# Kernel tuning notes

Measured on AMD Instinct MI355X. Metric: run time of the kernel, lower is better.

Reference implementation:

```python
import jax, jax.numpy as jnp
import numpy as np
import math

# dims: batch, tgt_len, img_feat, wordvec, heads, vocab, layers, ffn
N, T, D, W, H, V, L, FF = 8, 512, 1024, 512, 4, 32000, 2, 2048
NULL = 0  # padding_idx -> zero embedding row


def _pos_encoding(max_len, dim):
    pos = jnp.arange(max_len, dtype=jnp.float32)[:, None]
    j = jnp.arange(dim)[None, :]
    je = (j - (j % 2)).astype(jnp.float32)
    ang = pos * jnp.power(10000.0, -je / dim)
    return jnp.where(j % 2 == 0, jnp.sin(ang), jnp.cos(ang))  # (max_len, dim)


def setup_inputs() -> dict:
    key = jax.random.key(0)
    ks = iter(jax.random.split(key, 80))

    def nrm(shape):
        return jax.random.normal(next(ks), shape, jnp.float32) * 0.02

    inp = {}
    inp["features"] = jax.random.normal(next(ks), (N, D), jnp.float32)
    inp["captions"] = jax.random.randint(next(ks), (N, T), 0, V)
    emb = nrm((V, W)).at[NULL].set(0.0)  # padding_idx row zeroed
    inp["emb"] = emb
    inp["pe"] = _pos_encoding(T, W)
    inp["vis_w"] = nrm((D, W)); inp["vis_b"] = jnp.zeros((W,), jnp.float32)
    for p in ["sa", "ca"]:
        for q in ["q", "k", "v", "o"]:
            inp[f"{p}_w{q}"] = nrm((L, W, W))
            inp[f"{p}_b{q}"] = jnp.zeros((L, W), jnp.float32)
    inp["ff1_w"] = nrm((L, W, FF)); inp["ff1_b"] = jnp.zeros((L, FF), jnp.float32)
    inp["ff2_w"] = nrm((L, FF, W)); inp["ff2_b"] = jnp.zeros((L, W), jnp.float32)
    for i in (1, 2, 3):
        inp[f"ln{i}_w"] = jnp.ones((L, W), jnp.float32)
        inp[f"ln{i}_b"] = jnp.zeros((L, W), jnp.float32)
    inp["out_w"] = nrm((W, V)); inp["out_b"] = jnp.zeros((V,), jnp.float32)
    return inp


def _layer_norm(x, w, b):
    m = x.mean(-1, keepdims=True)
    v = ((x - m) ** 2).mean(-1, keepdims=True)
    return (x - m) / jnp.sqrt(v + 1e-5) * w + b


def _mha(qx, kx, vx, wq, bq, wk, bk, wv, bv, wo, bo, mask):
    n, s, e = qx.shape
    t = kx.shape[1]
    d = e // H
    q = (qx @ wq + bq).reshape(n, s, H, d)
    k = (kx @ wk + bk).reshape(n, t, H, d)
    v = (vx @ wv + bv).reshape(n, t, H, d)
    a = jnp.einsum("nshd,nthd->nhst", q, k) / math.sqrt(d)  # (N,H,S,T)
    if mask is not None:
        a = jnp.where(mask, a, -jnp.inf)
    e_ = jax.nn.softmax(a, axis=-1)
    y = jnp.einsum("nhst,nthd->nshd", e_, v).reshape(n, s, e)
    return y @ wo + bo


def reference(features, captions, emb, pe, vis_w, vis_b,
              sa_wq, sa_bq, sa_wk, sa_bk, sa_wv, sa_bv, sa_wo, sa_bo,
              ca_wq, ca_bq, ca_wk, ca_bk, ca_wv, ca_bv, ca_wo, ca_bo,
              ff1_w, ff1_b, ff2_w, ff2_b,
              ln1_w, ln1_b, ln2_w, ln2_b, ln3_w, ln3_b, out_w, out_b):
    memory = (features @ vis_w + vis_b)[:, None, :]  # (N,1,W)
    t_len = captions.shape[1]
    x = emb[captions] + pe[None, :t_len, :]  # (N,T,W)
    mask = jnp.tril(jnp.ones((t_len, t_len), bool))  # causal tgt_mask
    for l in range(L):
        t2 = _mha(x, x, x, sa_wq[l], sa_bq[l], sa_wk[l], sa_bk[l],
                  sa_wv[l], sa_bv[l], sa_wo[l], sa_bo[l], mask)
        x = _layer_norm(x + t2, ln1_w[l], ln1_b[l])
        t2 = _mha(x, memory, memory, ca_wq[l], ca_bq[l], ca_wk[l], ca_bk[l],
                  ca_wv[l], ca_bv[l], ca_wo[l], ca_bo[l], None)
        x = _layer_norm(x + t2, ln2_w[l], ln2_b[l])
        t2 = jax.nn.relu(x @ ff1_w[l] + ff1_b[l]) @ ff2_w[l] + ff2_b[l]
        x = _layer_norm(x + t2, ln3_w[l], ln3_b[l])
    return x @ out_w + out_b  # (N,T,V)
```

## Files before the change

### kernel.cpp

```cpp
#include <hip/hip_runtime.h>
#include <math.h>

#define WDIM   512
#define TLEN   512
#define NBATCH 8
#define NHEADS 4
#define DHEAD  128
#define VOCAB  32000
#define NLAY   2
#define FFDIM  2048
#define DFEAT  1024
#define NT     (NBATCH * TLEN)
#define QKVW   (3 * WDIM)

typedef unsigned short u16;
typedef __attribute__((ext_vector_type(8))) short bf16x8;
typedef __attribute__((ext_vector_type(4))) float f32x4;

__device__ inline u16 f2bf(float f) {
    union { float f; unsigned u; } v; v.f = f;
    unsigned r = v.u + 0x7fffu + ((v.u >> 16) & 1u);
    return (u16)(r >> 16);
}
__device__ inline u16 to_bf(float f) { return f2bf(f); }
__device__ inline u16 to_bf(u16 v)  { return v; }

__global__ __launch_bounds__(256)
void cvt_kernel(const float* __restrict__ s, u16* __restrict__ d, int n)
{
    int i = blockIdx.x * 256 + threadIdx.x;
    if (i < n) d[i] = f2bf(s[i]);
}

__global__ __launch_bounds__(256)
void concat_bias_kernel(const float* __restrict__ bq, const float* __restrict__ bk,
                        const float* __restrict__ bv, float* __restrict__ dst)
{
    int i = blockIdx.x * 256 + threadIdx.x;
    if (i >= NLAY * QKVW) return;
    int l = i / QKVW, j = i - l * QKVW;
    float v = (j < WDIM) ? bq[l * WDIM + j]
            : (j < 2 * WDIM) ? bk[l * WDIM + j - WDIM]
            : bv[l * WDIM + j - 2 * WDIM];
    dst[i] = v;
}

template<typename T>
__global__ __launch_bounds__(256)
void transpose_cvt_kernel(const T* __restrict__ src, int lds_, long ssn, long ssh,
                          u16* __restrict__ dst, int ldd, long dsn, long dsh,
                          int HH)
{
    int z = blockIdx.z;
    int zn = z / HH, zh = z - zn * HH;
    src += (long)zn * ssn + (long)zh * ssh;
    dst += (long)zn * dsn + (long)zh * dsh;
    __shared__ T tile[32][33];
    int n0 = blockIdx.x * 32, k0 = blockIdx.y * 32;
    int tx = threadIdx.x & 31, ty = threadIdx.x >> 5;
    #pragma unroll
    for (int i = 0; i < 32; i += 8)
        tile[ty + i][tx] = src[(long)(k0 + ty + i) * lds_ + n0 + tx];
    __syncthreads();
    #pragma unroll
    for (int i = 0; i < 32; i += 8)
        dst[(long)(n0 + ty + i) * ldd + k0 + tx] = to_bf(tile[tx][ty + i]);
}

__global__ __launch_bounds__(128)
void embed_kernel(const int* __restrict__ captions, const float* __restrict__ emb,
                  const float* __restrict__ pe, float* __restrict__ x, u16* __restrict__ xb)
{
    int r = blockIdx.x;
    int t = r % TLEN;
    int cap = captions[r];
    const float4* e4 = (const float4*)(emb + (long)cap * WDIM);
    const float4* p4 = (const float4*)(pe + (long)t * WDIM);
    float4 a = e4[threadIdx.x], b = p4[threadIdx.x];
    float4 o = make_float4(a.x + b.x, a.y + b.y, a.z + b.z, a.w + b.w);
    ((float4*)(x + (long)r * WDIM))[threadIdx.x] = o;
    ushort4 ob = make_ushort4(f2bf(o.x), f2bf(o.y), f2bf(o.z), f2bf(o.w));
    ((ushort4*)(xb + (long)r * WDIM))[threadIdx.x] = ob;
}

#define GBM 128
#define GBN 128
#define GBK 32

template<int RELU, int NTST, int CAUSAL>
__global__ __launch_bounds__(256)
void mfma_gemm_kernel(const u16* __restrict__ A, int lda, long sAn, long sAh,
                      const u16* __restrict__ B, int ldb, long sBn, long sBh,
                      float* __restrict__ C, u16* __restrict__ Cb, int ldc, long sCn, long sCh,
                      const float* __restrict__ bias,
                      int M, int N, int K, int HH, float alpha)
{
    int z = blockIdx.z;
    int zn = z / HH, zh = z - zn * HH;
    A += (long)zn * sAn + (long)zh * sAh;
    B += (long)zn * sBn + (long)zh * sBh;
    long coff = (long)zn * sCn + (long)zh * sCh;

    int nwg  = gridDim.x * gridDim.y;
    int orig = blockIdx.y * gridDim.x + blockIdx.x;
    int q = nwg >> 3, r = nwg & 7, xcd = orig & 7, rest = orig >> 3;
    int nw = (xcd < r ? xcd * (q + 1) : r * (q + 1) + (xcd - r) * q) + rest;
    int bx = nw / gridDim.y, by = nw - bx * gridDim.y;
    int bm = by * GBM, bn = bx * GBN;

    if (CAUSAL && bn >= bm + GBM) return;

    __shared__ u16 smem[2 * GBM * GBK];
    u16* As = smem;
    u16* Bs = smem + GBM * GBK;

    int tid = threadIdx.x;
    int w = tid >> 6, lane = tid & 63;
    int wr = w >> 1, wc = w & 1;
    int lrow = lane & 15, kgrp = lane >> 4;

    f32x4 acc[4][4] = {};

    for (int k0 = 0; k0 < K; k0 += GBK) {
        #pragma unroll
        for (int i = 0; i < 2; i++) {
            int c = tid + i * 256;
            int row = c >> 2, ko = (c & 3) << 3;
            int gr = bm + row; if (gr >= M) gr = M - 1;
            const u16* src = A + (long)gr * lda + k0 + ko;
            u16* dst = &As[(size_t)(w * 64 + i * 256) * 8];
            __builtin_amdgcn_global_load_lds((const __attribute__((address_space(1))) void*)src,
                                             (__attribute__((address_space(3))) void*)dst, 16, 0, 0);
        }
        #pragma unroll
        for (int i = 0; i < 2; i++) {
            int c = tid + i * 256;
            int row = c >> 2, ko = (c & 3) << 3;
            const u16* src = B + (long)(bn + row) * ldb + k0 + ko;
            u16* dst = &Bs[(size_t)(w * 64 + i * 256) * 8];
            __builtin_amdgcn_global_load_lds((const __attribute__((address_space(1))) void*)src,
                                             (__attribute__((address_space(3))) void*)dst, 16, 0, 0);
        }
        __syncthreads();
        bf16x8 av[4], bv[4];
        #pragma unroll
        for (int m = 0; m < 4; m++)
            av[m] = *(const bf16x8*)&As[(wr * 64 + m * 16 + lrow) * GBK + kgrp * 8];
        #pragma unroll
        for (int n = 0; n < 4; n++)
            bv[n] = *(const bf16x8*)&Bs[(wc * 64 + n * 16 + lrow) * GBK + kgrp * 8];
        #pragma unroll
        for (int m = 0; m < 4; m++)
            #pragma unroll
            for (int n = 0; n < 4; n++)
                acc[m][n] = __builtin_amdgcn_mfma_f32_16x16x32_bf16(av[m], bv[n], acc[m][n], 0, 0, 0);
        __syncthreads();
    }

    if (NTST) {
        float* ls = (float*)smem;
        C += coff;
        #pragma unroll
        for (int pass = 0; pass < 4; pass++) {
            if (wr == (pass >> 1)) {
                #pragma unroll
                for (int m2 = 0; m2 < 2; m2++) {
                    int m = (pass & 1) * 2 + m2;
                    #pragma unroll
                    for (int n = 0; n < 4; n++) {
                        int gc = wc * 64 + n * 16 + lrow;
                        float bvv = bias ? bias[bn + gc] : 0.f;
                        #pragma unroll
                        for (int r2 = 0; r2 < 4; r2++) {
                            float v2 = acc[m][n][r2] * alpha + bvv;
                            if (RELU) v2 = fmaxf(v2, 0.f);
                            ls[(m2 * 16 + kgrp * 4 + r2) * 128 + gc] = v2;
                        }
                    }
                }
            }
            __syncthreads();
            #pragma unroll
            for (int i = 0; i < 4; i++) {
                int j = tid + i * 256;
                int row = j >> 5, cg = j & 31;
                int gr = bm + pass * 32 + row;
                if (gr < M) {
                    f32x4 v4 = *(const f32x4*)&ls[row * 128 + cg * 4];
                    __builtin_nontemporal_store(v4, (f32x4*)&C[(long)gr * ldc + bn + cg * 4]);
                }
            }
            __syncthreads();
        }
        return;
    }

    if (C)  C  += coff;
    if (Cb) Cb += coff;
    #pragma unroll
    for (int m = 0; m < 4; m++) {
        int rb = bm + wr * 64 + m * 16 + kgrp * 4;
        #pragma unroll
        for (int n = 0; n < 4; n++) {
            int gc = bn + wc * 64 + n * 16 + lrow;
            float bvv = bias ? bias[gc] : 0.f;
            #pragma unroll
            for (int r2 = 0; r2 < 4; r2++) {
                int gr = rb + r2;
                if (gr < M) {
                    float v2 = acc[m][n][r2] * alpha + bvv;
                    if (RELU) v2 = fmaxf(v2, 0.f);
                    if (C)  C[(long)gr * ldc + gc]  = v2;
                    if (Cb) Cb[(long)gr * ldc + gc] = f2bf(v2);
                }
            }
        }
    }
}

__global__ __launch_bounds__(256)
void softmax_causal_kernel(const float* __restrict__ scores, u16* __restrict__ pb)
{
    long row = blockIdx.x;
    int s = (int)(row % TLEN);
    const float* p = scores + row * TLEN;
    u16* o = pb + row * TLEN;
    int tid = threadIdx.x;
    float v0 = p[tid], v1 = p[tid + 256];
    bool m0 = (tid <= s), m1 = (tid + 256 <= s);
    __shared__ float red[256];
    float mx = fmaxf(m0 ? v0 : -INFINITY, m1 ? v1 : -INFINITY);
    red[tid] = mx; __syncthreads();
    for (int off = 128; off > 0; off >>= 1) {
        if (tid < off) red[tid] = fmaxf(red[tid], red[tid + off]);
        __syncthreads();
    }
    mx = red[0]; __syncthreads();
    float e0 = m0 ? expf(v0 - mx) : 0.f;
    float e1 = m1 ? expf(v1 - mx) : 0.f;
    red[tid] = e0 + e1; __syncthreads();
    for (int off = 128; off > 0; off >>= 1) {
        if (tid < off) red[tid] += red[tid + off];
        __syncthreads();
    }
    float inv = 1.f / red[0];
    o[tid]       = f2bf(e0 * inv);
    o[tid + 256] = f2bf(e1 * inv);
}

__global__ __launch_bounds__(256)
void add_ln_kernel(float* __restrict__ x, u16* __restrict__ xb,
                   const float* __restrict__ t2, long t2div,
                   const float* __restrict__ w, const float* __restrict__ b)
{
    long r = blockIdx.x;
    float* xr = x + r * WDIM;
    u16* xbr = xb + r * WDIM;
    const float* tr = t2 + (r / t2div) * WDIM;
    int tid = threadIdx.x;
    float v0 = xr[tid] + tr[tid];
    float v1 = xr[tid + 256] + tr[tid + 256];
    __shared__ float red[256];
    red[tid] = v0 + v1; __syncthreads();
    for (int off = 128; off > 0; off >>= 1) {
        if (tid < off) red[tid] += red[tid + off];
        __syncthreads();
    }
    float mean = red[0] * (1.f / WDIM); __syncthreads();
    float d0 = v0 - mean, d1 = v1 - mean;
    red[tid] = d0 * d0 + d1 * d1; __syncthreads();
    for (int off = 128; off > 0; off >>= 1) {
        if (tid < off) red[tid] += red[tid + off];
        __syncthreads();
    }
    float rstd = 1.f / sqrtf(red[0] * (1.f / WDIM) + 1e-5f);
    float o0 = d0 * rstd * w[tid] + b[tid];
    float o1 = d1 * rstd * w[tid + 256] + b[tid + 256];
    xr[tid] = o0;        xr[tid + 256] = o1;
    xbr[tid] = f2bf(o0); xbr[tid + 256] = f2bf(o1);
}

extern "C" void kernel_launch(void* const* d_in, const int* in_sizes, int n_in,
                              void* d_out, int out_size, void* d_ws, size_t ws_size,
                              hipStream_t stream)
{
    const float* features = (const float*)d_in[0];
    const int*   captions = (const int*)  d_in[1];
    const float* emb      = (const float*)d_in[2];
    const float* pe       = (const float*)d_in[3];
    const float* vis_w    = (const float*)d_in[4];
    const float* vis_b    = (const float*)d_in[5];
    const float* sa_wq    = (const float*)d_in[6];
    const float* sa_bq    = (const float*)d_in[7];
    const float* sa_wk    = (const float*)d_in[8];
    const float* sa_bk    = (const float*)d_in[9];
    const float* sa_wv    = (const float*)d_in[10];
    const float* sa_bv    = (const float*)d_in[11];
    const float* sa_wo    = (const float*)d_in[12];
    const float* sa_bo    = (const float*)d_in[13];
    const float* ca_wv    = (const float*)d_in[18];
    const float* ca_bv    = (const float*)d_in[19];
    const float* ca_wo    = (const float*)d_in[20];
    const float* ca_bo    = (const float*)d_in[21];
    const float* ff1_w    = (const float*)d_in[22];
    const float* ff1_b    = (const float*)d_in[23];
    const float* ff2_w    = (const float*)d_in[24];
    const float* ff2_b    = (const float*)d_in[25];
    const float* ln1_w    = (const float*)d_in[26];
    const float* ln1_b    = (const float*)d_in[27];
    const float* ln2_w    = (const float*)d_in[28];
    const float* ln2_b    = (const float*)d_in[29];
    const float* ln3_w    = (const float*)d_in[30];
    const float* ln3_b    = (const float*)d_in[31];
    const float* out_w    = (const float*)d_in[32];
    const float* out_b    = (const float*)d_in[33];

    char* p = (char*)d_ws;
    auto alloc = [&](size_t bytes) { char* r = p; p += (bytes + 255) & ~(size_t)255; return r; };
    float* x    = (float*)alloc((size_t)NT * WDIM * 4);
    float* t2   = (float*)alloc((size_t)NT * WDIM * 4);
    float* memb = (float*)alloc((size_t)NBATCH * WDIM * 4);
    float* cav  = (float*)alloc((size_t)NBATCH * WDIM * 4);
    char*  reg1 = alloc((size_t)NBATCH * NHEADS * TLEN * TLEN * 4);
    float* scores = (float*)reg1;
    u16*   yb     = (u16*)reg1;
    u16*   hb     = (u16*)reg1;
    u16* xb    = (u16*)alloc((size_t)NT * WDIM * 2);
    u16* qkvb  = (u16*)alloc((size_t)NT * QKVW * 2);
    u16* vtb   = (u16*)alloc((size_t)NT * WDIM * 2);
    u16* pb    = (u16*)alloc((size_t)NBATCH * NHEADS * TLEN * TLEN * 2);
    u16* featb = (u16*)alloc((size_t)NBATCH * DFEAT * 2);
    u16* membf = (u16*)alloc((size_t)NBATCH * WDIM * 2);
    u16* cvb   = (u16*)alloc((size_t)NBATCH * WDIM * 2);
    float* qkv_bias = (float*)alloc((size_t)NLAY * QKVW * 4);
    u16* vis_wT = (u16*)alloc((size_t)WDIM * DFEAT * 2);
    u16* qkvT   = (u16*)alloc((size_t)NLAY * QKVW * WDIM * 2);
    u16* sa_woT = (u16*)alloc((size_t)NLAY * WDIM * WDIM * 2);
    u16* ca_wvT = (u16*)alloc((size_t)NLAY * WDIM * WDIM * 2);
    u16* ca_woT = (u16*)alloc((size_t)NLAY * WDIM * WDIM * 2);
    u16* ff1T   = (u16*)alloc((size_t)NLAY * WDIM * FFDIM * 2);
    u16* ff2T   = (u16*)alloc((size_t)NLAY * FFDIM * WDIM * 2);
    u16* out_wT = (u16*)alloc((size_t)WDIM * VOCAB * 2);

    auto gemm = [&](const u16* A, int lda, long sAn, long sAh,
                    const u16* B, int ldb, long sBn, long sBh,
                    float* C, u16* Cb, int ldc, long sCn, long sCh,
                    const float* bias, int M, int N, int K, int HH, int batch,
                    float alpha, int mode)
    {
        dim3 g(N / GBN, (M + GBM - 1) / GBM, batch), blk(256);
        if (mode == 2)
            mfma_gemm_kernel<0, 1, 0><<<g, blk, 0, stream>>>(A, lda, sAn, sAh, B, ldb, sBn, sBh,
                                                             C, Cb, ldc, sCn, sCh, bias, M, N, K, HH, alpha);
        else if (mode == 1)
            mfma_gemm_kernel<1, 0, 0><<<g, blk, 0, stream>>>(A, lda, sAn, sAh, B, ldb, sBn, sBh,
                                                             C, Cb, ldc, sCn, sCh, bias, M, N, K, HH, alpha);
        else if (mode == 3)
            mfma_gemm_kernel<0, 0, 1><<<g, blk, 0, stream>>>(A, lda, sAn, sAh, B, ldb, sBn, sBh,
                                                             C, Cb, ldc, sCn, sCh, bias, M, N, K, HH, alpha);
        else
            mfma_gemm_kernel<0, 0, 0><<<g, blk, 0, stream>>>(A, lda, sAn, sAh, B, ldb, sBn, sBh,
                                                             C, Cb, ldc, sCn, sCh, bias, M, N, K, HH, alpha);
    };
    auto transposeF = [&](const float* src, int lds_, long ssn, long ssh,
                          u16* dst, int ldd, long dsn, long dsh,
                          int K, int N, int batch, int HH)
    {
        dim3 g(N / 32, K / 32, batch), blk(256);
        transpose_cvt_kernel<float><<<g, blk, 0, stream>>>(src, lds_, ssn, ssh, dst, ldd, dsn, dsh, HH);
    };
    auto transposeB = [&](const u16* src, int lds_, long ssn, long ssh,
                          u16* dst, int ldd, long dsn, long dsh,
                          int K, int N, int batch, int HH)
    {
        dim3 g(N / 32, K / 32, batch), blk(256);
        transpose_cvt_kernel<u16><<<g, blk, 0, stream>>>(src, lds_, ssn, ssh, dst, ldd, dsn, dsh, HH);
    };

    cvt_kernel<<<(NBATCH * DFEAT + 255) / 256, 256, 0, stream>>>(features, featb, NBATCH * DFEAT);
    concat_bias_kernel<<<(NLAY * QKVW + 255) / 256, 256, 0, stream>>>(sa_bq, sa_bk, sa_bv, qkv_bias);
    transposeF(vis_w, WDIM, 0, 0, vis_wT, DFEAT, 0, 0, DFEAT, WDIM, 1, 1);
    transposeF(sa_wq, WDIM, (long)WDIM * WDIM, 0, qkvT,                WDIM, (long)QKVW * WDIM, 0, WDIM, WDIM, NLAY, 1);
    transposeF(sa_wk, WDIM, (long)WDIM * WDIM, 0, qkvT + (long)WDIM * WDIM,     WDIM, (long)QKVW * WDIM, 0, WDIM, WDIM, NLAY, 1);
    transposeF(sa_wv, WDIM, (long)WDIM * WDIM, 0, qkvT + (long)2 * WDIM * WDIM, WDIM, (long)QKVW * WDIM, 0, WDIM, WDIM, NLAY, 1);
    transposeF(sa_wo, WDIM, (long)WDIM * WDIM, 0, sa_woT, WDIM, (long)WDIM * WDIM, 0, WDIM, WDIM, NLAY, 1);
    transposeF(ca_wv, WDIM, (long)WDIM * WDIM, 0, ca_wvT, WDIM, (long)WDIM * WDIM, 0, WDIM, WDIM, NLAY, 1);
    transposeF(ca_wo, WDIM, (long)WDIM * WDIM, 0, ca_woT, WDIM, (long)WDIM * WDIM, 0, WDIM, WDIM, NLAY, 1);
    transposeF(ff1_w, FFDIM, (long)WDIM * FFDIM, 0, ff1T, WDIM, (long)FFDIM * WDIM, 0, WDIM, FFDIM, NLAY, 1);
    transposeF(ff2_w, WDIM, (long)FFDIM * WDIM, 0, ff2T, FFDIM, (long)WDIM * FFDIM, 0, FFDIM, WDIM, NLAY, 1);
    transposeF(out_w, VOCAB, 0, 0, out_wT, WDIM, 0, 0, WDIM, VOCAB, 1, 1);

    gemm(featb, DFEAT, 0, 0, vis_wT, DFEAT, 0, 0, memb, membf, WDIM, 0, 0,
         vis_b, NBATCH, WDIM, DFEAT, 1, 1, 1.f, 0);
    embed_kernel<<<NT, 128, 0, stream>>>(captions, emb, pe, x, xb);

    const float iscale = 1.f / sqrtf((float)DHEAD);
    const long TQ = (long)TLEN * QKVW;
    const long TW = (long)TLEN * WDIM;
    const long TT = (long)TLEN * TLEN;
    for (int l = 0; l < NLAY; l++) {
        long wo  = (long)l * WDIM * WDIM;
        long bo_ = (long)l * WDIM;
        gemm(xb, WDIM, 0, 0, qkvT + (long)l * QKVW * WDIM, WDIM, 0, 0,
             nullptr, qkvb, QKVW, 0, 0, qkv_bias + (long)l * QKVW,
             NT, QKVW, WDIM, 1, 1, 1.f, 0);
        transposeB(qkvb + 2 * WDIM, QKVW, TQ, DHEAD,
                   vtb, TLEN, (long)NHEADS * DHEAD * TLEN, (long)DHEAD * TLEN,
                   TLEN, DHEAD, NBATCH * NHEADS, NHEADS);
        gemm(qkvb, QKVW, TQ, DHEAD, qkvb + WDIM, QKVW, TQ, DHEAD,
             scores, nullptr, TLEN, (long)NHEADS * TT, TT,
             nullptr, TLEN, TLEN, DHEAD, NHEADS, NBATCH * NHEADS, iscale, 3);
        softmax_causal_kernel<<<NBATCH * NHEADS * TLEN, 256, 0, stream>>>(scores, pb);
        gemm(pb, TLEN, (long)NHEADS * TT, TT,
             vtb, TLEN, (long)NHEADS * DHEAD * TLEN, (long)DHEAD * TLEN,
             nullptr, yb, WDIM, TW, DHEAD,
             nullptr, TLEN, DHEAD, TLEN, NHEADS, NBATCH * NHEADS, 1.f, 0);
        gemm(yb, WDIM, 0, 0, sa_woT + wo, WDIM, 0, 0, t2, nullptr, WDIM, 0, 0,
             sa_bo + bo_, NT, WDIM, WDIM, 1, 1, 1.f, 0);
        add_ln_kernel<<<NT, 256, 0, stream>>>(x, xb, t2, 1, ln1_w + bo_, ln1_b + bo_);
        gemm(membf, WDIM, 0, 0, ca_wvT + wo, WDIM, 0, 0, nullptr, cvb, WDIM, 0, 0,
             ca_bv + bo_, NBATCH, WDIM, WDIM, 1, 1, 1.f, 0);
        gemm(cvb, WDIM, 0, 0, ca_woT + wo, WDIM, 0, 0, cav, nullptr, WDIM, 0, 0,
             ca_bo + bo_, NBATCH, WDIM, WDIM, 1, 1, 1.f, 0);
        add_ln_kernel<<<NT, 256, 0, stream>>>(x, xb, cav, TLEN, ln2_w + bo_, ln2_b + bo_);
        gemm(xb, WDIM, 0, 0, ff1T + (long)l * FFDIM * WDIM, WDIM, 0, 0,
             nullptr, hb, FFDIM, 0, 0, ff1_b + (long)l * FFDIM,
             NT, FFDIM, WDIM, 1, 1, 1.f, 1);
        gemm(hb, FFDIM, 0, 0, ff2T + (long)l * WDIM * FFDIM, FFDIM, 0, 0,
             t2, nullptr, WDIM, 0, 0, ff2_b + bo_, NT, WDIM, FFDIM, 1, 1, 1.f, 0);
        add_ln_kernel<<<NT, 256, 0, stream>>>(x, xb, t2, 1, ln3_w + bo_, ln3_b + bo_);
    }
    gemm(xb, WDIM, 0, 0, out_wT, WDIM, 0, 0, (float*)d_out, nullptr, VOCAB, 0, 0,
         out_b, NT, VOCAB, WDIM, 1, 1, 1.f, 2);
}
```

Measured before the change: 823.4 us.

## Double-buffer LDS tiles in the bf16 GEMM to overlap loads with MFMA

Splits the shared-memory A/B tiles into two buffers. The next K-step's global-to-LDS loads are issued before the MFMAs on the current buffer, so load latency can overlap with compute instead of sitting behind a barrier each step. The store epilogue reuses the first buffer region as float scratch. LDS use per block doubles, which may lower occupancy.

```diff
diff --git a/kernel.cpp b/kernel.cpp
--- a/kernel.cpp
+++ b/kernel.cpp
@@ -110,45 +110,50 @@
 
     if (CAUSAL && bn >= bm + GBM) return;
 
-    __shared__ u16 smem[2 * GBM * GBK];
-    u16* As = smem;
-    u16* Bs = smem + GBM * GBK;
+    __shared__ u16 As[2][GBM * GBK];
+    __shared__ u16 Bs[2][GBN * GBK];
 
     int tid = threadIdx.x;
     int w = tid >> 6, lane = tid & 63;
     int wr = w >> 1, wc = w & 1;
     int lrow = lane & 15, kgrp = lane >> 4;
 
+    int c0row = tid >> 2, c0ko = (tid & 3) << 3;
+    long ldsOff = (size_t)(w * 64) * 8;
+
+    auto STAGE = [&](int buf, int ks) {
+        int k0 = ks * GBK;
+        #pragma unroll
+        for (int i = 0; i < 2; i++) {
+            int row = c0row + i * 64;
+            int gr = bm + row; if (gr >= M) gr = M - 1;
+            const u16* srcA = A + (long)gr * lda + k0 + c0ko;
+            u16* dstA = &As[buf][ldsOff + (size_t)i * 256 * 8];
+            __builtin_amdgcn_global_load_lds((const __attribute__((address_space(1))) void*)srcA,
+                                             (__attribute__((address_space(3))) void*)dstA, 16, 0, 0);
+            const u16* srcB = B + (long)(bn + row) * ldb + k0 + c0ko;
+            u16* dstB = &Bs[buf][ldsOff + (size_t)i * 256 * 8];
+            __builtin_amdgcn_global_load_lds((const __attribute__((address_space(1))) void*)srcB,
+                                             (__attribute__((address_space(3))) void*)dstB, 16, 0, 0);
+        }
+    };
+
     f32x4 acc[4][4] = {};
-
-    for (int k0 = 0; k0 < K; k0 += GBK) {
-        #pragma unroll
-        for (int i = 0; i < 2; i++) {
-            int c = tid + i * 256;
-            int row = c >> 2, ko = (c & 3) << 3;
-            int gr = bm + row; if (gr >= M) gr = M - 1;
-            const u16* src = A + (long)gr * lda + k0 + ko;
-            u16* dst = &As[(size_t)(w * 64 + i * 256) * 8];
-            __builtin_amdgcn_global_load_lds((const __attribute__((address_space(1))) void*)src,
-                                             (__attribute__((address_space(3))) void*)dst, 16, 0, 0);
-        }
-        #pragma unroll
-        for (int i = 0; i < 2; i++) {
-            int c = tid + i * 256;
-            int row = c >> 2, ko = (c & 3) << 3;
-            const u16* src = B + (long)(bn + row) * ldb + k0 + ko;
-            u16* dst = &Bs[(size_t)(w * 64 + i * 256) * 8];
-            __builtin_amdgcn_global_load_lds((const __attribute__((address_space(1))) void*)src,
-                                             (__attribute__((address_space(3))) void*)dst, 16, 0, 0);
-        }
-        __syncthreads();
+    int nsteps = K / GBK;
+
+    STAGE(0, 0);
+    __syncthreads();
+
+    for (int ks = 0; ks < nsteps; ks++) {
+        int cur = ks & 1;
+        if (ks + 1 < nsteps) STAGE(cur ^ 1, ks + 1);
         bf16x8 av[4], bv[4];
         #pragma unroll
         for (int m = 0; m < 4; m++)
-            av[m] = *(const bf16x8*)&As[(wr * 64 + m * 16 + lrow) * GBK + kgrp * 8];
+            av[m] = *(const bf16x8*)&As[cur][(wr * 64 + m * 16 + lrow) * GBK + kgrp * 8];
         #pragma unroll
         for (int n = 0; n < 4; n++)
-            bv[n] = *(const bf16x8*)&Bs[(wc * 64 + n * 16 + lrow) * GBK + kgrp * 8];
+            bv[n] = *(const bf16x8*)&Bs[cur][(wc * 64 + n * 16 + lrow) * GBK + kgrp * 8];
         #pragma unroll
         for (int m = 0; m < 4; m++)
             #pragma unroll
@@ -158,7 +163,7 @@
     }
 
     if (NTST) {
-        float* ls = (float*)smem;
+        float* ls = (float*)&As[0][0];
         C += coff;
         #pragma unroll
         for (int pass = 0; pass < 4; pass++) {
```

New measurement: 772.0 us. 6.2% less time.
